# Optimization experiments

Measured on AMD Instinct MI355X. Metric: run time of the kernel, lower is better.

## Reference

```python
import jax, jax.numpy as jnp
import numpy as np

WORD_LEN = 4094
MAX_LEN = 9
EMB = 512
HID = 256
BATCH = 32768


def setup_inputs() -> dict:
    key = jax.random.key(0)
    ks = jax.random.split(key, 16)
    s = 0.02
    return {
        "decode_word": jax.random.randint(ks[0], (BATCH, 1), 0, WORD_LEN),
        "hidden": jax.random.normal(ks[1], (BATCH, HID), jnp.float32),
        "encoder_output": jax.random.normal(ks[2], (BATCH, MAX_LEN, HID), jnp.float32),
        "emb_table": jax.random.normal(ks[3], (WORD_LEN, EMB), jnp.float32) * s,
        "atten_W": jax.random.normal(ks[4], (MAX_LEN, 2 * HID), jnp.float32) * s,
        "atten_b": jnp.zeros((MAX_LEN,), jnp.float32),
        "comb_W": jax.random.normal(ks[5], (EMB, EMB + HID), jnp.float32) * s,
        "comb_b": jnp.zeros((EMB,), jnp.float32),
        "W_ih": jax.random.normal(ks[6], (3 * HID, EMB), jnp.float32) * s,
        "b_ih": jnp.zeros((3 * HID,), jnp.float32),
        "W_hh": jax.random.normal(ks[7], (3 * HID, HID), jnp.float32) * s,
        "b_hh": jnp.zeros((3 * HID,), jnp.float32),
        "out_W": jax.random.normal(ks[8], (WORD_LEN, HID), jnp.float32) * s,
        "out_b": jnp.zeros((WORD_LEN,), jnp.float32),
    }


def reference(decode_word, hidden, encoder_output, emb_table, atten_W, atten_b,
              comb_W, comb_b, W_ih, b_ih, W_hh, b_hh, out_W, out_b):
    # embedding: [B,1,E]
    embedded = emb_table[decode_word]
    B = hidden.shape[0]
    # expand hidden to [B,L,H], concat with encoder_output -> attention scores [B,L,L]
    hx = jnp.broadcast_to(hidden[:, None, :], (B, MAX_LEN, HID))
    scores = jnp.einsum('blf,mf->blm', jnp.concatenate([encoder_output, hx], axis=2), atten_W) + atten_b
    atten_weight = jax.nn.softmax(scores, axis=2)
    # bmm: [B,L,L] @ [B,L,H] -> [B,L,H], then sum over L -> context [B,1,H]
    atten_applied = jnp.einsum('blm,bmh->blh', atten_weight, encoder_output)
    c_i = atten_applied.sum(axis=1)[:, None, :]
    # combine + relu: [B,1,E]
    x = jnp.concatenate([embedded, c_i], axis=2) @ comb_W.T + comb_b
    x = jax.nn.relu(x)[:, 0]  # [B,E]
    # GRUCell (PyTorch gate order: r, z, n)
    gi = x @ W_ih.T + b_ih
    gh = hidden @ W_hh.T + b_hh
    i_r, i_z, i_n = jnp.split(gi, 3, axis=1)
    h_r, h_z, h_n = jnp.split(gh, 3, axis=1)
    r = jax.nn.sigmoid(i_r + h_r)
    z = jax.nn.sigmoid(i_z + h_z)
    n = jnp.tanh(i_n + r * h_n)
    h_new = (1.0 - z) * n + z * hidden
    # output projection + log_softmax over vocab
    out = jax.nn.log_softmax(h_new @ out_W.T + out_b, axis=1)
    return out, h_new
```

## Files before the change

kernel.cpp:

```cpp
#include <hip/hip_runtime.h>

typedef __bf16 bf16x8 __attribute__((ext_vector_type(8)));
typedef float  f32x4  __attribute__((ext_vector_type(4)));

#define BATCH_ 32768
#define VOC 4094
#define LGT_STRIDE 8188

__device__ inline unsigned short f2bf(float f) {
    unsigned int u = __builtin_bit_cast(unsigned int, f);
    unsigned int r = u + 0x7FFFu + ((u >> 16) & 1u);
    return (unsigned short)(r >> 16);
}
__device__ inline float bf2f(unsigned short u) {
    unsigned int v = ((unsigned int)u) << 16;
    return __builtin_bit_cast(float, v);
}
__device__ inline f32x4 mfma16(bf16x8 a, bf16x8 b, f32x4 c) {
    return __builtin_amdgcn_mfma_f32_16x16x32_bf16(a, b, c, 0, 0, 0);
}
__device__ inline void gload16(const void* g, void* l) {
    __builtin_amdgcn_global_load_lds(
        (const __attribute__((address_space(1))) void*)(g),
        (__attribute__((address_space(3))) void*)(l),
        16, 0, 0);
}

__global__ __launch_bounds__(256) void k_prep(
    const float* __restrict__ comb_W, const float* __restrict__ W_ih,
    const float* __restrict__ W_hh, const float* __restrict__ out_W,
    const float* __restrict__ b_ih, const float* __restrict__ b_hh,
    const float* __restrict__ out_b,
    unsigned short* __restrict__ cwb, unsigned short* __restrict__ wg2,
    unsigned short* __restrict__ owb, float* __restrict__ bg,
    float* __restrict__ obp) {
    int i = blockIdx.x * 256 + threadIdx.x;
    if (i < 512 * 768) {
        int n = i / 768, k = i - n * 768;
        int by = n >> 7, r = n & 127, kc = k >> 6, kl = k & 63;
        int dst = (by * 12 + kc) * 8192 + r * 64 + (((kl >> 3) ^ (r & 7)) << 3) + (kl & 7);
        cwb[dst] = f2bf(comb_W[i]);
    }
    if (i < 1024 * 768) {
        int row = i / 768, k = i - row * 768;
        int hgrp = row >> 6, g = (row >> 4) & 3, hl = row & 15;
        int h = hgrp * 16 + hl;
        float v;
        if (g == 0) v = (k < 512) ? W_ih[(size_t)h * 512 + k] : W_hh[(size_t)h * 256 + (k - 512)];
        else if (g == 1) v = (k < 512) ? W_ih[(size_t)(256 + h) * 512 + k] : W_hh[(size_t)(256 + h) * 256 + (k - 512)];
        else if (g == 2) v = (k < 512) ? W_ih[(size_t)(512 + h) * 512 + k] : 0.f;
        else v = (k < 512) ? 0.f : W_hh[(size_t)(512 + h) * 256 + (k - 512)];
        int by = row >> 7, r = row & 127, kc = k >> 6, kl = k & 63;
        int dst = (by * 12 + kc) * 8192 + r * 64 + (((kl >> 3) ^ (r & 7)) << 3) + (kl & 7);
        wg2[dst] = f2bf(v);
    }
    if (i < 4096 * 256) {
        int n = i >> 8, k = i & 255;
        int by = n >> 7, r = n & 127, kc = k >> 6, kl = k & 63;
        int dst = (by * 4 + kc) * 8192 + r * 64 + (((kl >> 3) ^ (r & 7)) << 3) + (kl & 7);
        owb[dst] = (n < VOC) ? f2bf(out_W[i]) : (unsigned short)0;
    }
    if (i < 1024) {
        float v = (i < 512) ? (b_ih[i] + b_hh[i]) : ((i < 768) ? b_ih[i] : b_hh[i - 256]);
        bg[i] = v;
    }
    if (i < 4096) obp[i] = (i < VOC) ? out_b[i] : -1.0e30f;
}

__global__ __launch_bounds__(256) void k_attn(
    const int* __restrict__ dw, const float* __restrict__ hidden,
    const float* __restrict__ enc, const float* __restrict__ emb,
    const float* __restrict__ aW, const float* __restrict__ ab,
    unsigned short* __restrict__ xcat, unsigned short* __restrict__ xh) {
    __shared__ float sAW[9 * 516];
    __shared__ float sAB[9];
    int tid = threadIdx.x;
    for (int i = tid; i < 9 * 512; i += 256) {
        int m = i >> 9, k = i & 511;
        sAW[m * 516 + k] = aW[i];
    }
    if (tid < 9) sAB[tid] = ab[tid];
    __syncthreads();
    int w = tid >> 6, lane = tid & 63;
    int b = blockIdx.x * 4 + w;
    const float* encb = enc + (size_t)b * (9 * 256);
    float4 h4 = *(const float4*)(hidden + (size_t)b * 256 + 4 * lane);

    float4 e[9];
#pragma unroll
    for (int l = 0; l < 9; l++) e[l] = *(const float4*)(encb + l * 256 + 4 * lane);

    float u[9];
#pragma unroll
    for (int m = 0; m < 9; m++) {
        float4 a = *(const float4*)&sAW[m * 516 + 256 + 4 * lane];
        float v = h4.x * a.x + h4.y * a.y + h4.z * a.z + h4.w * a.w;
        v += __shfl_xor(v, 1);  v += __shfl_xor(v, 2);  v += __shfl_xor(v, 4);
        v += __shfl_xor(v, 8);  v += __shfl_xor(v, 16); v += __shfl_xor(v, 32);
        u[m] = v + sAB[m];
    }
    float wsum[9] = {0, 0, 0, 0, 0, 0, 0, 0, 0};
#pragma unroll
    for (int l = 0; l < 9; l++) {
        float p[9];
#pragma unroll
        for (int m = 0; m < 9; m++) {
            float4 a = *(const float4*)&sAW[m * 516 + 4 * lane];
            float v = e[l].x * a.x + e[l].y * a.y + e[l].z * a.z + e[l].w * a.w;
            v += __shfl_xor(v, 1);  v += __shfl_xor(v, 2);  v += __shfl_xor(v, 4);
            v += __shfl_xor(v, 8);  v += __shfl_xor(v, 16); v += __shfl_xor(v, 32);
            p[m] = v + u[m];
        }
        float mx = p[0];
#pragma unroll
        for (int m = 1; m < 9; m++) mx = fmaxf(mx, p[m]);
        float s = 0.f, ex[9];
#pragma unroll
        for (int m = 0; m < 9; m++) { ex[m] = __expf(p[m] - mx); s += ex[m]; }
        float inv = 1.f / s;
#pragma unroll
        for (int m = 0; m < 9; m++) wsum[m] += ex[m] * inv;
    }
    float c0 = 0, c1 = 0, c2 = 0, c3 = 0;
#pragma unroll
    for (int m = 0; m < 9; m++) {
        c0 += wsum[m] * e[m].x; c1 += wsum[m] * e[m].y;
        c2 += wsum[m] * e[m].z; c3 += wsum[m] * e[m].w;
    }
    ushort4 cb; cb.x = f2bf(c0); cb.y = f2bf(c1); cb.z = f2bf(c2); cb.w = f2bf(c3);
    *(ushort4*)(xcat + (size_t)b * 768 + 512 + 4 * lane) = cb;
    ushort4 hb; hb.x = f2bf(h4.x); hb.y = f2bf(h4.y); hb.z = f2bf(h4.z); hb.w = f2bf(h4.w);
    *(ushort4*)(xh + (size_t)b * 768 + 512 + 4 * lane) = hb;

    int word = dw[b];
    const float* er = emb + (size_t)word * 512 + 8 * lane;
    float4 e0 = *(const float4*)er;
    float4 e1 = *(const float4*)(er + 4);
    ushort4 w0; w0.x = f2bf(e0.x); w0.y = f2bf(e0.y); w0.z = f2bf(e0.z); w0.w = f2bf(e0.w);
    ushort4 w1; w1.x = f2bf(e1.x); w1.y = f2bf(e1.y); w1.z = f2bf(e1.z); w1.w = f2bf(e1.w);
    *(ushort4*)(xcat + (size_t)b * 768 + 8 * lane) = w0;
    *(ushort4*)(xcat + (size_t)b * 768 + 8 * lane + 4) = w1;
}

__global__ __launch_bounds__(256, 4) void k_combine(
    const unsigned short* __restrict__ xcat, const unsigned short* __restrict__ cwb,
    const float* __restrict__ comb_b, unsigned short* __restrict__ xh) {
    __shared__ __align__(16) char smem[32768];
    int wgid = blockIdx.x;
    int xcd = wgid & 7, slot = wgid >> 3;
    int bx = xcd * 32 + (slot & 31), by = slot >> 5;
    int tid = threadIdx.x, w = tid >> 6, lane = tid & 63;
    int lo = lane & 15, hi = lane >> 4;
    int bm0 = bx * 128, n0 = by * 128;
    const __bf16* A = (const __bf16*)xcat;
    const char* gb = (const char*)cwb + (size_t)by * 12 * 16384;
    size_t ar = (size_t)(bm0 + w * 32 + lo) * 768 + 8 * hi;
    f32x4 acc[2][8] = {};
    bf16x8 Afb[2][2][2];
#pragma unroll
    for (int mf = 0; mf < 2; mf++)
#pragma unroll
        for (int ks = 0; ks < 2; ks++)
            Afb[0][mf][ks] = *(const bf16x8*)(A + ar + mf * 16 * 768 + ks * 32);
    for (int it = 0; it < 4; it++) {
        int uo = (w * 4 + it) << 10;
        gload16(gb + uo + lane * 16, smem + uo);
    }
    __syncthreads();
#pragma unroll
    for (int c = 0; c < 12; c++) {
        int cur = c & 1;
        if (c < 11) {
            const char* gc = gb + (size_t)(c + 1) * 16384;
            char* lb = smem + (cur ^ 1) * 16384;
            for (int it = 0; it < 4; it++) {
                int uo = (w * 4 + it) << 10;
                gload16(gc + uo + lane * 16, lb + uo);
            }
#pragma unroll
            for (int mf = 0; mf < 2; mf++)
#pragma unroll
                for (int ks = 0; ks < 2; ks++)
                    Afb[cur ^ 1][mf][ks] = *(const bf16x8*)(A + ar + mf * 16 * 768 + (c + 1) * 64 + ks * 32);
        }
        const char* cb = smem + cur * 16384;
#pragma unroll
        for (int ks = 0; ks < 2; ks++)
#pragma unroll
            for (int nf = 0; nf < 8; nf++) {
                int row = nf * 16 + lo;
                bf16x8 bfr = *(const bf16x8*)(cb + row * 128 + (((ks * 4 + hi) ^ (lo & 7)) << 4));
                acc[0][nf] = mfma16(Afb[cur][0][ks], bfr, acc[0][nf]);
                acc[1][nf] = mfma16(Afb[cur][1][ks], bfr, acc[1][nf]);
            }
        __syncthreads();
    }
#pragma unroll
    for (int mf = 0; mf < 2; mf++)
#pragma unroll
        for (int nf = 0; nf < 8; nf++) {
            int col = n0 + nf * 16 + lo;
            float cb = comb_b[col];
#pragma unroll
            for (int r = 0; r < 4; r++) {
                int row = bm0 + w * 32 + mf * 16 + hi * 4 + r;
                xh[(size_t)row * 768 + col] = f2bf(fmaxf(acc[mf][nf][r] + cb, 0.f));
            }
        }
}

__global__ __launch_bounds__(256, 4) void k_gru(
    const unsigned short* __restrict__ xh, const unsigned short* __restrict__ wg2,
    const float* __restrict__ bg, const float* __restrict__ hidden,
    float* __restrict__ hnew_out, unsigned short* __restrict__ hnb) {
    __shared__ __align__(16) char smem[32768];
    int wgid = blockIdx.x;
    int xcd = wgid & 7, slot = wgid >> 3;
    int bx = xcd * 32 + (slot & 31), by = slot >> 5;
    int tid = threadIdx.x, w = tid >> 6, lane = tid & 63;
    int lo = lane & 15, hi = lane >> 4;
    int bm0 = bx * 128;
    int h00 = by * 32;
    const __bf16* A = (const __bf16*)xh;
    const char* gb = (const char*)wg2 + (size_t)by * 12 * 16384;
    size_t ar = (size_t)(bm0 + w * 32 + lo) * 768 + 8 * hi;
    f32x4 acc[2][8] = {};
    bf16x8 Afb[2][2][2];
#pragma unroll
    for (int mf = 0; mf < 2; mf++)
#pragma unroll
        for (int ks = 0; ks < 2; ks++)
            Afb[0][mf][ks] = *(const bf16x8*)(A + ar + mf * 16 * 768 + ks * 32);
    for (int it = 0; it < 4; it++) {
        int uo = (w * 4 + it) << 10;
        gload16(gb + uo + lane * 16, smem + uo);
    }
    __syncthreads();
#pragma unroll
    for (int c = 0; c < 12; c++) {
        int cur = c & 1;
        if (c < 11) {
            const char* gc = gb + (size_t)(c + 1) * 16384;
            char* lb = smem + (cur ^ 1) * 16384;
            for (int it = 0; it < 4; it++) {
                int uo = (w * 4 + it) << 10;
                gload16(gc + uo + lane * 16, lb + uo);
            }
#pragma unroll
            for (int mf = 0; mf < 2; mf++)
#pragma unroll
                for (int ks = 0; ks < 2; ks++)
                    Afb[cur ^ 1][mf][ks] = *(const bf16x8*)(A + ar + mf * 16 * 768 + (c + 1) * 64 + ks * 32);
        }
        const char* cb = smem + cur * 16384;
#pragma unroll
        for (int ks = 0; ks < 2; ks++)
#pragma unroll
            for (int nf = 0; nf < 8; nf++) {
                int row = nf * 16 + lo;
                bf16x8 bfr = *(const bf16x8*)(cb + row * 128 + (((ks * 4 + hi) ^ (lo & 7)) << 4));
                acc[0][nf] = mfma16(Afb[cur][0][ks], bfr, acc[0][nf]);
                acc[1][nf] = mfma16(Afb[cur][1][ks], bfr, acc[1][nf]);
            }
        __syncthreads();
    }
#pragma unroll
    for (int mf = 0; mf < 2; mf++)
#pragma unroll
        for (int hgrp = 0; hgrp < 2; hgrp++) {
            int col = h00 + hgrp * 16 + lo;
            float br = bg[col], bz = bg[256 + col], bi = bg[512 + col], bh = bg[768 + col];
#pragma unroll
            for (int r = 0; r < 4; r++) {
                int row = bm0 + w * 32 + mf * 16 + hi * 4 + r;
                float rr = 1.f / (1.f + __expf(-(acc[mf][hgrp * 4 + 0][r] + br)));
                float zz = 1.f / (1.f + __expf(-(acc[mf][hgrp * 4 + 1][r] + bz)));
                float nn = tanhf(acc[mf][hgrp * 4 + 2][r] + bi + rr * (acc[mf][hgrp * 4 + 3][r] + bh));
                float hp = hidden[(size_t)row * 256 + col];
                float hn = zz * (hp - nn) + nn;
                hnew_out[(size_t)row * 256 + col] = hn;
                hnb[(size_t)row * 256 + col] = f2bf(hn);
            }
        }
}

__global__ __launch_bounds__(256, 4) void k_logit(
    const unsigned short* __restrict__ hnb, const unsigned short* __restrict__ owb,
    const float* __restrict__ obp, unsigned short* __restrict__ lgt,
    float* __restrict__ psum) {
    __shared__ __align__(16) char smem[34816];
    int wgid = blockIdx.x;
    int xcd = wgid & 7, slot = wgid >> 3;
    int bx = xcd * 32 + (slot & 31), by = slot >> 5;
    int tid = threadIdx.x, w = tid >> 6, lane = tid & 63;
    int lo = lane & 15, hi = lane >> 4;
    int bm0 = bx * 128, n0 = by * 128;
    const __bf16* A = (const __bf16*)hnb;
    const char* gb = (const char*)owb + (size_t)by * 4 * 16384;
    size_t ar = (size_t)(bm0 + w * 32 + lo) * 256 + 8 * hi;
    f32x4 acc[2][8] = {};
    bf16x8 Afb[2][2][2];
#pragma unroll
    for (int mf = 0; mf < 2; mf++)
#pragma unroll
        for (int ks = 0; ks < 2; ks++)
            Afb[0][mf][ks] = *(const bf16x8*)(A + ar + mf * 16 * 256 + ks * 32);
    for (int it = 0; it < 4; it++) {
        int uo = (w * 4 + it) << 10;
        gload16(gb + uo + lane * 16, smem + uo);
    }
    __syncthreads();
#pragma unroll
    for (int c = 0; c < 4; c++) {
        int cur = c & 1;
        if (c < 3) {
            const char* gc = gb + (size_t)(c + 1) * 16384;
            char* lb = smem + (cur ^ 1) * 16384;
            for (int it = 0; it < 4; it++) {
                int uo = (w * 4 + it) << 10;
                gload16(gc + uo + lane * 16, lb + uo);
            }
#pragma unroll
            for (int mf = 0; mf < 2; mf++)
#pragma unroll
                for (int ks = 0; ks < 2; ks++)
                    Afb[cur ^ 1][mf][ks] = *(const bf16x8*)(A + ar + mf * 16 * 256 + (c + 1) * 64 + ks * 32);
        }
        const char* cb = smem + cur * 16384;
#pragma unroll
        for (int ks = 0; ks < 2; ks++)
#pragma unroll
            for (int nf = 0; nf < 8; nf++) {
                int row = nf * 16 + lo;
                bf16x8 bfr = *(const bf16x8*)(cb + row * 128 + (((ks * 4 + hi) ^ (lo & 7)) << 4));
                acc[0][nf] = mfma16(Afb[cur][0][ks], bfr, acc[0][nf]);
                acc[1][nf] = mfma16(Afb[cur][1][ks], bfr, acc[1][nf]);
            }
        __syncthreads();
    }

    unsigned short* T = (unsigned short*)smem;
    float se[2][4] = {};
#pragma unroll
    for (int mf = 0; mf < 2; mf++)
#pragma unroll
        for (int nf = 0; nf < 8; nf++) {
            int col = n0 + nf * 16 + lo;
            float ob = obp[col];
#pragma unroll
            for (int r = 0; r < 4; r++) {
                float lg = acc[mf][nf][r] + ob;
                se[mf][r] += __expf(lg);
                T[(w * 32 + mf * 16 + hi * 4 + r) * 136 + nf * 16 + lo] = f2bf(lg);
            }
        }
#pragma unroll
    for (int mf = 0; mf < 2; mf++)
#pragma unroll
        for (int r = 0; r < 4; r++) {
            float v = se[mf][r];
            v += __shfl_xor(v, 1); v += __shfl_xor(v, 2);
            v += __shfl_xor(v, 4); v += __shfl_xor(v, 8);
            se[mf][r] = v;
        }
    if (lo == 0) {
#pragma unroll
        for (int mf = 0; mf < 2; mf++)
#pragma unroll
            for (int r = 0; r < 4; r++)
                psum[(size_t)by * BATCH_ + bm0 + w * 32 + mf * 16 + hi * 4 + r] = se[mf][r];
    }
    __syncthreads();
#pragma unroll
    for (int it = 0; it < 8; it++) {
        int t = it * 256 + tid;
        int row = t >> 4, ch = t & 15;
        ushort4 a = *(ushort4*)(T + row * 136 + ch * 8);
        ushort4 b = *(ushort4*)(T + row * 136 + ch * 8 + 4);
        size_t base = (size_t)(bm0 + row) * LGT_STRIDE + n0 + ch * 8;
        *(ushort4*)(lgt + base) = a;
        *(ushort4*)(lgt + base + 4) = b;
    }
}

__global__ __launch_bounds__(256) void k_out2(
    const float* __restrict__ psum, float* __restrict__ out) {
    __shared__ float sl;
    int b = blockIdx.x, tid = threadIdx.x;
    const unsigned short* rowp = (const unsigned short*)(out + (size_t)b * VOC);
    ushort4 a0 = *(const ushort4*)(rowp + tid * 8);
    ushort4 b0 = *(const ushort4*)(rowp + tid * 8 + 4);
    ushort4 a1 = *(const ushort4*)(rowp + 2048 + tid * 8);
    ushort4 b1 = *(const ushort4*)(rowp + 2048 + tid * 8 + 4);
    if (tid < 32) {
        float v = psum[(size_t)tid * BATCH_ + b];
        v += __shfl_xor(v, 1); v += __shfl_xor(v, 2); v += __shfl_xor(v, 4);
        v += __shfl_xor(v, 8); v += __shfl_xor(v, 16);
        if (tid == 0) sl = __logf(v);
    }
    __syncthreads();
    float l = sl;
    float* orow = out + (size_t)b * VOC;
    int v0 = tid * 8;
    {
        float2 p;
        p.x = bf2f(a0.x) - l; p.y = bf2f(a0.y) - l; *(float2*)(orow + v0) = p;
        p.x = bf2f(a0.z) - l; p.y = bf2f(a0.w) - l; *(float2*)(orow + v0 + 2) = p;
        p.x = bf2f(b0.x) - l; p.y = bf2f(b0.y) - l; *(float2*)(orow + v0 + 4) = p;
        p.x = bf2f(b0.z) - l; p.y = bf2f(b0.w) - l; *(float2*)(orow + v0 + 6) = p;
    }
    int v1 = 2048 + tid * 8;
    {
        float2 p;
        p.x = bf2f(a1.x) - l; p.y = bf2f(a1.y) - l;
        if (v1 + 1 < VOC) *(float2*)(orow + v1) = p;
        p.x = bf2f(a1.z) - l; p.y = bf2f(a1.w) - l;
        if (v1 + 3 < VOC) *(float2*)(orow + v1 + 2) = p;
        p.x = bf2f(b1.x) - l; p.y = bf2f(b1.y) - l;
        if (v1 + 5 < VOC) *(float2*)(orow + v1 + 4) = p;
        p.x = bf2f(b1.z) - l; p.y = bf2f(b1.w) - l;
        if (v1 + 7 < VOC) *(float2*)(orow + v1 + 6) = p;
    }
}

extern "C" void kernel_launch(void* const* d_in, const int* in_sizes, int n_in,
                              void* d_out, int out_size, void* d_ws, size_t ws_size,
                              hipStream_t stream) {
    const int*   dw      = (const int*)d_in[0];
    const float* hidden  = (const float*)d_in[1];
    const float* enc     = (const float*)d_in[2];
    const float* emb     = (const float*)d_in[3];
    const float* aW      = (const float*)d_in[4];
    const float* ab      = (const float*)d_in[5];
    const float* comb_W  = (const float*)d_in[6];
    const float* comb_b  = (const float*)d_in[7];
    const float* W_ih    = (const float*)d_in[8];
    const float* b_ih    = (const float*)d_in[9];
    const float* W_hh    = (const float*)d_in[10];
    const float* b_hh    = (const float*)d_in[11];
    const float* out_W   = (const float*)d_in[12];
    const float* out_b   = (const float*)d_in[13];

    float* out = (float*)d_out;
    float* hnew_out = out + (size_t)BATCH_ * VOC;

    unsigned short* xcat = (unsigned short*)d_ws;
    unsigned short* xh   = xcat + (size_t)BATCH_ * 768;
    unsigned short* hnb  = xh + (size_t)BATCH_ * 768;
    float* psum          = (float*)(hnb + (size_t)BATCH_ * 256);
    float* obp           = psum + (size_t)32 * BATCH_;
    unsigned short* cwb  = (unsigned short*)(obp + 4096);
    unsigned short* wg2  = cwb + 512 * 768;
    unsigned short* owb  = wg2 + 1024 * 768;
    float* bg            = (float*)(owb + 4096 * 256);

    k_prep<<<4096, 256, 0, stream>>>(comb_W, W_ih, W_hh, out_W, b_ih, b_hh, out_b,
                                     cwb, wg2, owb, bg, obp);
    k_attn<<<BATCH_ / 4, 256, 0, stream>>>(dw, hidden, enc, emb, aW, ab, xcat, xh);
    k_combine<<<1024, 256, 0, stream>>>(xcat, cwb, comb_b, xh);
    k_gru<<<2048, 256, 0, stream>>>(xh, wg2, bg, hidden, hnew_out, hnb);
    k_logit<<<8192, 256, 0, stream>>>(hnb, owb, obp, (unsigned short*)out, psum);
    k_out2<<<BATCH_, 256, 0, stream>>>(psum, out);
}
```

Measured before the change: 760.2 us.

## Compute attention scores with bf16 MFMA over 64-row batch tiles

The attention kernel now processes 64 batch rows per block and computes the 9-way attention scores for both encoder and hidden halves with 16x16x32 bf16 MFMA, replacing per-wave shuffle reductions. Softmax weights are reduced through shared-memory atomics, then a second pass re-reads encoder rows to form the context vector and converts hidden and embeddings to bf16. This removes heavy shuffle/FMA work but rounds scores to bf16 and reads the encoder tensor twice, with uncoalesced per-thread strided access in the second pass.

Result: slower. 984.0 us (+29.4%).

```diff
diff --git a/kernel.cpp b/kernel.cpp
--- a/kernel.cpp
+++ b/kernel.cpp
@@ -1,6 +1,7 @@
 #include <hip/hip_runtime.h>
 
 typedef __bf16 bf16x8 __attribute__((ext_vector_type(8)));
+typedef unsigned short u16x8 __attribute__((ext_vector_type(8)));
 typedef float  f32x4  __attribute__((ext_vector_type(4)));
 
 #define BATCH_ 32768
@@ -24,6 +25,12 @@
         (const __attribute__((address_space(1))) void*)(g),
         (__attribute__((address_space(3))) void*)(l),
         16, 0, 0);
+}
+__device__ inline bf16x8 pack8(float4 a, float4 b) {
+    u16x8 u;
+    u[0] = f2bf(a.x); u[1] = f2bf(a.y); u[2] = f2bf(a.z); u[3] = f2bf(a.w);
+    u[4] = f2bf(b.x); u[5] = f2bf(b.y); u[6] = f2bf(b.z); u[7] = f2bf(b.w);
+    return __builtin_bit_cast(bf16x8, u);
 }
 
 __global__ __launch_bounds__(256) void k_prep(
@@ -72,74 +79,126 @@
     const float* __restrict__ enc, const float* __restrict__ emb,
     const float* __restrict__ aW, const float* __restrict__ ab,
     unsigned short* __restrict__ xcat, unsigned short* __restrict__ xh) {
-    __shared__ float sAW[9 * 516];
-    __shared__ float sAB[9];
-    int tid = threadIdx.x;
-    for (int i = tid; i < 9 * 512; i += 256) {
-        int m = i >> 9, k = i & 511;
-        sAW[m * 516 + k] = aW[i];
-    }
-    if (tid < 9) sAB[tid] = ab[tid];
-    __syncthreads();
-    int w = tid >> 6, lane = tid & 63;
-    int b = blockIdx.x * 4 + w;
-    const float* encb = enc + (size_t)b * (9 * 256);
-    float4 h4 = *(const float4*)(hidden + (size_t)b * 256 + 4 * lane);
-
-    float4 e[9];
-#pragma unroll
-    for (int l = 0; l < 9; l++) e[l] = *(const float4*)(encb + l * 256 + 4 * lane);
-
-    float u[9];
-#pragma unroll
-    for (int m = 0; m < 9; m++) {
-        float4 a = *(const float4*)&sAW[m * 516 + 256 + 4 * lane];
-        float v = h4.x * a.x + h4.y * a.y + h4.z * a.z + h4.w * a.w;
-        v += __shfl_xor(v, 1);  v += __shfl_xor(v, 2);  v += __shfl_xor(v, 4);
-        v += __shfl_xor(v, 8);  v += __shfl_xor(v, 16); v += __shfl_xor(v, 32);
-        u[m] = v + sAB[m];
-    }
-    float wsum[9] = {0, 0, 0, 0, 0, 0, 0, 0, 0};
-#pragma unroll
-    for (int l = 0; l < 9; l++) {
-        float p[9];
+    __shared__ __align__(16) unsigned short sA1[16 * 264];
+    __shared__ __align__(16) unsigned short sA2[16 * 264];
+    __shared__ float sU[64][17];
+    __shared__ float sW[64][17];
+    __shared__ float sAB[16];
+    int tid = threadIdx.x, w = tid >> 6, lane = tid & 63;
+    int lo = lane & 15, hi = lane >> 4;
+    int B0 = blockIdx.x * 64;
+
+    for (int i = tid; i < 16 * 256; i += 256) {
+        int m = i >> 8, k = i & 255;
+        float v1 = (m < 9) ? aW[m * 512 + k] : 0.f;
+        float v2 = (m < 9) ? aW[m * 512 + 256 + k] : 0.f;
+        sA1[m * 264 + k] = f2bf(v1);
+        sA2[m * 264 + k] = f2bf(v2);
+    }
+    if (tid < 16) sAB[tid] = (tid < 9) ? ab[tid] : 0.f;
+    if (tid < 64) {
+#pragma unroll
+        for (int m = 0; m < 16; m++) sW[tid][m] = 0.f;
+    }
+    __syncthreads();
+
+    {
+        const float* hrow = hidden + (size_t)(B0 + w * 16 + lo) * 256 + 8 * hi;
+        f32x4 uacc = {};
+#pragma unroll
+        for (int ks = 0; ks < 8; ks++) {
+            float4 f0 = *(const float4*)(hrow + ks * 32);
+            float4 f1 = *(const float4*)(hrow + ks * 32 + 4);
+            bf16x8 Bf = pack8(f0, f1);
+            bf16x8 Af = *(const bf16x8*)(sA2 + lo * 264 + ks * 32 + 8 * hi);
+            uacc = mfma16(Af, Bf, uacc);
+        }
+#pragma unroll
+        for (int r = 0; r < 4; r++) {
+            int m = hi * 4 + r;
+            sU[w * 16 + lo][m] = uacc[r] + sAB[m];
+        }
+    }
+    __syncthreads();
+
+    bf16x8 Asc[8];
+#pragma unroll
+    for (int ks = 0; ks < 8; ks++)
+        Asc[ks] = *(const bf16x8*)(sA1 + lo * 264 + ks * 32 + 8 * hi);
+    const float* encF = enc + (size_t)B0 * 9 * 256;
+#pragma unroll
+    for (int t = 0; t < 9; t++) {
+        int rowloc = w * 144 + t * 16 + lo;
+        const float* er = encF + (size_t)rowloc * 256 + 8 * hi;
+        f32x4 acc = {};
+#pragma unroll
+        for (int ks = 0; ks < 8; ks++) {
+            float4 f0 = *(const float4*)(er + ks * 32);
+            float4 f1 = *(const float4*)(er + ks * 32 + 4);
+            bf16x8 Bf = pack8(f0, f1);
+            acc = mfma16(Asc[ks], Bf, acc);
+        }
+        int bloc = rowloc / 9;
+        float s[4];
+        float mx = -1.0e30f;
+#pragma unroll
+        for (int r = 0; r < 4; r++) {
+            int m = hi * 4 + r;
+            s[r] = acc[r] + sU[bloc][m];
+            if (m < 9) mx = fmaxf(mx, s[r]);
+        }
+        mx = fmaxf(mx, __shfl_xor(mx, 16));
+        mx = fmaxf(mx, __shfl_xor(mx, 32));
+        float ex[4], sm = 0.f;
+#pragma unroll
+        for (int r = 0; r < 4; r++) {
+            int m = hi * 4 + r;
+            ex[r] = (m < 9) ? __expf(s[r] - mx) : 0.f;
+            sm += ex[r];
+        }
+        sm += __shfl_xor(sm, 16);
+        sm += __shfl_xor(sm, 32);
+        float inv = 1.f / sm;
+#pragma unroll
+        for (int r = 0; r < 4; r++) {
+            int m = hi * 4 + r;
+            if (m < 9) atomicAdd(&sW[bloc][m], ex[r] * inv);
+        }
+    }
+    __syncthreads();
+
+    int b = tid >> 2, q = tid & 3;
+    float ws[9];
+#pragma unroll
+    for (int m = 0; m < 9; m++) ws[m] = sW[b][m];
+    const float* encB = enc + (size_t)(B0 + b) * 9 * 256 + q * 64;
+    const float* hp = hidden + (size_t)(B0 + b) * 256 + q * 64;
+    unsigned short* xc = xcat + (size_t)(B0 + b) * 768 + 512 + q * 64;
+    unsigned short* xhp = xh + (size_t)(B0 + b) * 768 + 512 + q * 64;
+#pragma unroll
+    for (int g = 0; g < 16; g++) {
+        float4 c = {0.f, 0.f, 0.f, 0.f};
 #pragma unroll
         for (int m = 0; m < 9; m++) {
-            float4 a = *(const float4*)&sAW[m * 516 + 4 * lane];
-            float v = e[l].x * a.x + e[l].y * a.y + e[l].z * a.z + e[l].w * a.w;
-            v += __shfl_xor(v, 1);  v += __shfl_xor(v, 2);  v += __shfl_xor(v, 4);
-            v += __shfl_xor(v, 8);  v += __shfl_xor(v, 16); v += __shfl_xor(v, 32);
-            p[m] = v + u[m];
-        }
-        float mx = p[0];
-#pragma unroll
-        for (int m = 1; m < 9; m++) mx = fmaxf(mx, p[m]);
-        float s = 0.f, ex[9];
-#pragma unroll
-        for (int m = 0; m < 9; m++) { ex[m] = __expf(p[m] - mx); s += ex[m]; }
-        float inv = 1.f / s;
-#pragma unroll
-        for (int m = 0; m < 9; m++) wsum[m] += ex[m] * inv;
-    }
-    float c0 = 0, c1 = 0, c2 = 0, c3 = 0;
-#pragma unroll
-    for (int m = 0; m < 9; m++) {
-        c0 += wsum[m] * e[m].x; c1 += wsum[m] * e[m].y;
-        c2 += wsum[m] * e[m].z; c3 += wsum[m] * e[m].w;
-    }
-    ushort4 cb; cb.x = f2bf(c0); cb.y = f2bf(c1); cb.z = f2bf(c2); cb.w = f2bf(c3);
-    *(ushort4*)(xcat + (size_t)b * 768 + 512 + 4 * lane) = cb;
-    ushort4 hb; hb.x = f2bf(h4.x); hb.y = f2bf(h4.y); hb.z = f2bf(h4.z); hb.w = f2bf(h4.w);
-    *(ushort4*)(xh + (size_t)b * 768 + 512 + 4 * lane) = hb;
-
-    int word = dw[b];
-    const float* er = emb + (size_t)word * 512 + 8 * lane;
-    float4 e0 = *(const float4*)er;
-    float4 e1 = *(const float4*)(er + 4);
-    ushort4 w0; w0.x = f2bf(e0.x); w0.y = f2bf(e0.y); w0.z = f2bf(e0.z); w0.w = f2bf(e0.w);
-    ushort4 w1; w1.x = f2bf(e1.x); w1.y = f2bf(e1.y); w1.z = f2bf(e1.z); w1.w = f2bf(e1.w);
-    *(ushort4*)(xcat + (size_t)b * 768 + 8 * lane) = w0;
-    *(ushort4*)(xcat + (size_t)b * 768 + 8 * lane + 4) = w1;
+            float4 e4 = *(const float4*)(encB + m * 256 + g * 4);
+            c.x += ws[m] * e4.x; c.y += ws[m] * e4.y;
+            c.z += ws[m] * e4.z; c.w += ws[m] * e4.w;
+        }
+        ushort4 cb; cb.x = f2bf(c.x); cb.y = f2bf(c.y); cb.z = f2bf(c.z); cb.w = f2bf(c.w);
+        *(ushort4*)(xc + g * 4) = cb;
+        float4 h4 = *(const float4*)(hp + g * 4);
+        ushort4 hb; hb.x = f2bf(h4.x); hb.y = f2bf(h4.y); hb.z = f2bf(h4.z); hb.w = f2bf(h4.w);
+        *(ushort4*)(xhp + g * 4) = hb;
+    }
+    int word = dw[B0 + b];
+    const float* er2 = emb + (size_t)word * 512 + q * 128;
+    unsigned short* xe = xcat + (size_t)(B0 + b) * 768 + q * 128;
+#pragma unroll
+    for (int g = 0; g < 32; g++) {
+        float4 e4 = *(const float4*)(er2 + g * 4);
+        ushort4 eb; eb.x = f2bf(e4.x); eb.y = f2bf(e4.y); eb.z = f2bf(e4.z); eb.w = f2bf(e4.w);
+        *(ushort4*)(xe + g * 4) = eb;
+    }
 }
 
 __global__ __launch_bounds__(256, 4) void k_combine(
@@ -456,7 +515,7 @@
 
     k_prep<<<4096, 256, 0, stream>>>(comb_W, W_ih, W_hh, out_W, b_ih, b_hh, out_b,
                                      cwb, wg2, owb, bg, obp);
-    k_attn<<<BATCH_ / 4, 256, 0, stream>>>(dw, hidden, enc, emb, aW, ab, xcat, xh);
+    k_attn<<<BATCH_ / 64, 256, 0, stream>>>(dw, hidden, enc, emb, aW, ab, xcat, xh);
     k_combine<<<1024, 256, 0, stream>>>(xcat, cwb, comb_b, xh);
     k_gru<<<2048, 256, 0, stream>>>(xh, wg2, bg, hidden, hnew_out, hnb);
     k_logit<<<8192, 256, 0, stream>>>(hnb, owb, obp, (unsigned short*)out, psum);
```
